# Performance work log

Measured on AMD Instinct MI355X. Metric: run time of the kernel, lower is better.

## Reference

```python
import jax, jax.numpy as jnp
import numpy as np

N, E, H, F, ED, IN = 50000, 800000, 4, 32, 5, 256
NEG_SLOPE = 0.2


def setup_inputs() -> dict:
    key = jax.random.key(0)
    ks = jax.random.split(key, 13)
    s = 0.05
    return {
        "feat": jax.random.normal(ks[0], (N, IN), jnp.float32),
        "edge_fea": jax.random.normal(ks[1], (E, ED), jnp.float32),
        "src": jax.random.randint(ks[2], (E,), 0, N, dtype=jnp.int32),
        "dst": jax.random.randint(ks[3], (E,), 0, N, dtype=jnp.int32),
        "W_fc": jax.random.normal(ks[4], (IN, H * F), jnp.float32) * s,
        "W_edg": jax.random.normal(ks[5], (ED, H * ED), jnp.float32) * s,
        "b_edg": jnp.zeros((H * ED,), jnp.float32),
        "attn_l": jax.random.normal(ks[6], (1, H, F), jnp.float32) * s,
        "attn_r": jax.random.normal(ks[7], (1, H, F), jnp.float32) * s,
        "attn_edg": jax.random.normal(ks[8], (1, H, ED), jnp.float32) * s,
        "W_out": jax.random.normal(ks[9], (ED + F, F), jnp.float32) * s,
        "b_out": jnp.zeros((F,), jnp.float32),
        "bias": jnp.zeros((H * F,), jnp.float32),
    }


def reference(feat, edge_fea, src, dst, W_fc, W_edg, b_edg,
              attn_l, attn_r, attn_edg, W_out, b_out, bias):
    # node projection: [N, IN] -> [N, H, F]
    feat_src = (feat @ W_fc).reshape(N, H, F)
    # edge projection: [E, ED] -> [E, H, ED]
    efe = (edge_fea @ W_edg + b_edg).reshape(E, H, ED)
    # per-head attention logits
    el = (feat_src * attn_l).sum(-1)          # [N, H]
    er = (feat_src * attn_r).sum(-1)          # [N, H]
    ee = (efe * attn_edg).sum(-1)             # [E, H]
    e = jax.nn.leaky_relu(el[src] + er[dst] + ee, NEG_SLOPE)  # [E, H]
    # edge softmax over incoming edges of each dst node (numerically stable)
    m = jax.ops.segment_max(e, dst, num_segments=N)            # [N, H]
    ex = jnp.exp(e - m[dst])
    den = jax.ops.segment_sum(ex, dst, num_segments=N)         # [N, H]
    a = (ex / den[dst])[:, :, None]                            # [E, H, 1]
    # two weighted scatter-aggregations
    ft_f = jax.ops.segment_sum(a * efe, dst, num_segments=N)             # [N, H, ED]
    ft = jax.ops.segment_sum(a * feat_src[src], dst, num_segments=N)     # [N, H, F]
    rst = jnp.concatenate([ft_f, ft], axis=-1) @ W_out + b_out           # [N, H, F]
    rst = rst + bias.reshape(1, H, F)
    return rst
```

## Files before the change

### kernel.cpp

```cpp
#include <hip/hip_runtime.h>
#include <hip/hip_fp16.h>

#define N_NODES 50000
#define E_EDGES 800000
#define H_HEADS 4
#define F_FEAT 32
#define ED_DIM 5
#define IN_DIM 256
#define HF 128
#define NEG_SLOPE 0.2f
#define MAXD 64
#define PAYD 48
#define NPB 16
#define PROJ_BLOCKS 782
#define SCAT_BLOCKS 3125

typedef _Float16 half8 __attribute__((ext_vector_type(8)));
typedef float floatx4 __attribute__((ext_vector_type(4)));

__global__ __launch_bounds__(64) void k_wconv(
    const float* __restrict__ W_fc,
    const float* __restrict__ W_edg, const float* __restrict__ b_edg,
    const float* __restrict__ attn_edg,
    _Float16* __restrict__ Whi, _Float16* __restrict__ Wlo,
    float* __restrict__ WAc, int* __restrict__ cnt)
{
    int b = blockIdx.x;
    int l = threadIdx.x;
    for (int i = b * 64 + l; i < N_NODES; i += 64 * 64) cnt[i] = 0;
    if (b == 0 && l == 0) {
        for (int h = 0; h < 4; ++h) {
            float c0 = 0.f;
            for (int d = 0; d < 5; ++d) c0 += b_edg[h * 5 + d] * attn_edg[h * 5 + d];
            WAc[20 + h] = c0;
            for (int i = 0; i < 5; ++i) {
                float w = 0.f;
                for (int d = 0; d < 5; ++d) w += W_edg[i * 20 + h * 5 + d] * attn_edg[h * 5 + d];
                WAc[i * 4 + h] = w;
            }
        }
    }
    int kt = b >> 3, nt = b & 7;
    int kbase = kt * 32 + (l >> 4) * 8;
    int n = nt * 16 + (l & 15);
    half8 hi, lo;
#pragma unroll
    for (int j = 0; j < 8; ++j) {
        float w = W_fc[(kbase + j) * HF + n];
        _Float16 h = (_Float16)w;
        hi[j] = h;
        lo[j] = (_Float16)(w - (float)h);
    }
    size_t off = ((size_t)b * 64 + l) * 8;
    *(half8*)(Whi + off) = hi;
    *(half8*)(Wlo + off) = lo;
}

template <bool PAY>
__global__ __launch_bounds__(256) void k_proj_scatter(
    const float* __restrict__ feat,
    const _Float16* __restrict__ Whi,
    const _Float16* __restrict__ Wlo,
    const float* __restrict__ attn_l,
    const float* __restrict__ attn_r,
    const int* __restrict__ dst,
    const int* __restrict__ src,
    const float* __restrict__ edge_fea,
    const float* __restrict__ WAc,
    __half2* __restrict__ feat_src,
    float* __restrict__ el,
    float* __restrict__ er,
    int* __restrict__ cnt,
    int* __restrict__ slots,
    char* __restrict__ pay)
{
    if (blockIdx.x >= PROJ_BLOCKS) {
        int e = (blockIdx.x - PROJ_BLOCKS) * 256 + threadIdx.x;
        if (e < E_EDGES) {
            int d = dst[e];
            if constexpr (PAY) {
                int s = src[e];
                const float* ep = edge_fea + (size_t)e * 5;
                float ef0 = ep[0], ef1 = ep[1], ef2 = ep[2], ef3 = ep[3], ef4 = ep[4];
                float ee0 = WAc[20] + ef0*WAc[0] + ef1*WAc[4]  + ef2*WAc[8]  + ef3*WAc[12] + ef4*WAc[16];
                float ee1 = WAc[21] + ef0*WAc[1] + ef1*WAc[5]  + ef2*WAc[9]  + ef3*WAc[13] + ef4*WAc[17];
                float ee2 = WAc[22] + ef0*WAc[2] + ef1*WAc[6]  + ef2*WAc[10] + ef3*WAc[14] + ef4*WAc[18];
                float ee3 = WAc[23] + ef0*WAc[3] + ef1*WAc[7]  + ef2*WAc[11] + ef3*WAc[15] + ef4*WAc[19];
                int pos = atomicAdd(&cnt[d], 1);
                if (pos < PAYD) {
                    float4* pb = (float4*)(pay + ((size_t)d * PAYD + pos) * 32);
                    pb[0] = make_float4(ef0, ef1, ef2, ef3);
                    __half2 e01 = __floats2half2_rn(ee0, ee1);
                    __half2 e23 = __floats2half2_rn(ee2, ee3);
                    float4 w2;
                    w2.x = ef4;
                    w2.y = __int_as_float(s);
                    w2.z = __uint_as_float(*(unsigned*)&e01);
                    w2.w = __uint_as_float(*(unsigned*)&e23);
                    pb[1] = w2;
                }
            } else {
                int pos = atomicAdd(&cnt[d], 1);
                if (pos < MAXD) slots[(size_t)d * MAXD + pos] = e;
            }
        }
        return;
    }

    __shared__ _Float16 sC[4][16][136];

    int t = threadIdx.x;
    int lane = t & 63, wv = t >> 6;
    int l15 = lane & 15, lq = lane >> 4;
    int n0 = blockIdx.x * 64 + wv * 16;
    int arow = n0 + l15;
    int ar = arow < N_NODES ? arow : 0;

    floatx4 acc[8];
#pragma unroll
    for (int i = 0; i < 8; ++i) acc[i] = (floatx4){0.f, 0.f, 0.f, 0.f};

    const float4* Arow = (const float4*)(feat + (size_t)ar * IN_DIM);
    const half8* BH = (const half8*)Whi;
    const half8* BL = (const half8*)Wlo;
    int abase = lq * 2;

    for (int ks = 0; ks < 8; ++ks) {
        float4 a0 = Arow[ks * 8 + abase];
        float4 a1 = Arow[ks * 8 + abase + 1];
        float av[8] = {a0.x, a0.y, a0.z, a0.w, a1.x, a1.y, a1.z, a1.w};
        half8 ahi, alo;
#pragma unroll
        for (int j = 0; j < 8; ++j) {
            _Float16 h = (_Float16)av[j];
            ahi[j] = h;
            alo[j] = (_Float16)(av[j] - (float)h);
        }
#pragma unroll
        for (int tt = 0; tt < 8; ++tt) {
            half8 bh = BH[(ks * 8 + tt) * 64 + lane];
            half8 bl = BL[(ks * 8 + tt) * 64 + lane];
            acc[tt] = __builtin_amdgcn_mfma_f32_16x16x32_f16(ahi, bh, acc[tt], 0, 0, 0);
            acc[tt] = __builtin_amdgcn_mfma_f32_16x16x32_f16(alo, bh, acc[tt], 0, 0, 0);
            acc[tt] = __builtin_amdgcn_mfma_f32_16x16x32_f16(ahi, bl, acc[tt], 0, 0, 0);
        }
    }

#pragma unroll
    for (int tt = 0; tt < 8; ++tt) {
        int c = tt * 16 + l15;
#pragma unroll
        for (int r = 0; r < 4; ++r)
            sC[wv][lq * 4 + r][c] = (_Float16)acc[tt][r];
    }
    __syncthreads();

    int lr = lane >> 2;
    int hh = lane & 3;
    int n = n0 + lr;
    const _Float16* crow = &sC[wv][lr][hh * 32];
    const float* alp = attn_l + hh * 32;
    const float* arp = attn_r + hh * 32;
    float pl = 0.f, pr = 0.f;
#pragma unroll
    for (int i = 0; i < 32; ++i) {
        float v = (float)crow[i];
        pl += v * alp[i];
        pr += v * arp[i];
    }
    if (n < N_NODES) {
        el[n * H_HEADS + hh] = pl;
        er[n * H_HEADS + hh] = pr;
        uint4* po = (uint4*)(feat_src + (size_t)n * 64 + hh * 16);
        const uint4* ps = (const uint4*)crow;
        po[0] = ps[0]; po[1] = ps[1]; po[2] = ps[2]; po[3] = ps[3];
    }
}

__device__ __forceinline__ void acc8f(float* acc, uint4 v, float a) {
    float2 f;
    f = __half22float2(*(__half2*)&v.x); acc[0] += a * f.x; acc[1] += a * f.y;
    f = __half22float2(*(__half2*)&v.y); acc[2] += a * f.x; acc[3] += a * f.y;
    f = __half22float2(*(__half2*)&v.z); acc[4] += a * f.x; acc[5] += a * f.y;
    f = __half22float2(*(__half2*)&v.w); acc[6] += a * f.x; acc[7] += a * f.y;
}

template <bool PAY>
__global__ __launch_bounds__(256) void k_gather_out(
    const int* __restrict__ cnt, const int* __restrict__ slots,
    const char* __restrict__ pay,
    const int* __restrict__ src,
    const float* __restrict__ edge_fea,
    const float* __restrict__ el, const float* __restrict__ er,
    const __half2* __restrict__ feat_src,
    const float* __restrict__ W_edg, const float* __restrict__ b_edg,
    const float* __restrict__ attn_edg,
    const float* __restrict__ W_out, const float* __restrict__ b_out,
    const float* __restrict__ bias,
    float* __restrict__ out)
{
    constexpr int PD   = PAY ? PAYD : MAXD;
    constexpr int SAVR = PAY ? 200  : 264;
    constexpr int SSR  = PAY ? 50   : 66;

    __shared__ float sWe[100], sBe[20], sA[20], sWo[37 * 32], sBo[32], sBi[128];
    __shared__ __align__(16) __half          sav[NPB * SAVR];
    __shared__ __align__(16) unsigned short ssrc[NPB * SSR];
    __shared__ __align__(16) __half          sft[NPB * 136];
    int t = threadIdx.x;
    if (t < 100) sWe[t] = W_edg[t];
    if (t < 20) { sBe[t] = b_edg[t]; sA[t] = attn_edg[t]; }
    for (int i = t; i < 37 * 32; i += 256) sWo[i] = W_out[i];
    if (t < 32)  sBo[t] = b_out[t];
    if (t < 128) sBi[t] = bias[t];
    __syncthreads();

    int lane = t & 63;
    int wv   = t >> 6;
    int q    = lane >> 4;
    int ql   = lane & 15;
    int nb   = wv * 4 + q;
    int n    = blockIdx.x * NPB + nb;
    int h    = ql >> 2;

    int dq = cnt[n]; if (dq > PD) dq = PD;

    if (ql == 0) ssrc[nb * SSR] = 0;
    if (ql < 4)  sav[nb * SAVR + ql] = __float2half(0.f);

    float4 ern = ((const float4*)er)[n];

    float WA[5][4], cst[4];
    if constexpr (!PAY) {
#pragma unroll
        for (int hh = 0; hh < 4; hh++) {
            float c0 = 0.f;
#pragma unroll
            for (int dd = 0; dd < 5; dd++) c0 += sBe[hh * 5 + dd] * sA[hh * 5 + dd];
            cst[hh] = c0;
#pragma unroll
            for (int i = 0; i < 5; i++) {
                float w = 0.f;
#pragma unroll
                for (int dd = 0; dd < 5; dd++) w += sWe[i * 20 + hh * 5 + dd] * sA[hh * 5 + dd];
                WA[i][hh] = w;
            }
        }
    }

    int dmax = dq;
    { int o = __shfl_xor(dmax, 16); dmax = dmax > o ? dmax : o;
      o = __shfl_xor(dmax, 32);     dmax = dmax > o ? dmax : o; }

    float sa4[4] = {0.f, 0.f, 0.f, 0.f};
    float m[20];
#pragma unroll
    for (int i = 0; i < 20; i++) m[i] = 0.f;

    for (int r = 0; r < dmax; r += 16) {
        int idx = r + ql;
        if (idx < dq) {
            float ef0, ef1, ef2, ef3, ef4;
            float b0, b1, b2, b3;
            int s;
            if constexpr (PAY) {
                const uint4* pb = (const uint4*)pay + ((size_t)n * PAYD + idx) * 2;
                uint4 p0 = pb[0], p1 = pb[1];
                ef0 = __uint_as_float(p0.x); ef1 = __uint_as_float(p0.y);
                ef2 = __uint_as_float(p0.z); ef3 = __uint_as_float(p0.w);
                ef4 = __uint_as_float(p1.x);
                s   = (int)p1.y;
                __half2 e01 = *(__half2*)&p1.z;
                __half2 e23 = *(__half2*)&p1.w;
                float2 f01 = __half22float2(e01);
                float2 f23 = __half22float2(e23);
                b0 = f01.x; b1 = f01.y; b2 = f23.x; b3 = f23.y;
            } else {
                int e = slots[(size_t)n * MAXD + idx];
                s = src[e];
                const float* ep = edge_fea + (size_t)e * 5;
                ef0 = ep[0]; ef1 = ep[1]; ef2 = ep[2]; ef3 = ep[3]; ef4 = ep[4];
                b0 = cst[0] + ef0*WA[0][0] + ef1*WA[1][0] + ef2*WA[2][0] + ef3*WA[3][0] + ef4*WA[4][0];
                b1 = cst[1] + ef0*WA[0][1] + ef1*WA[1][1] + ef2*WA[2][1] + ef3*WA[3][1] + ef4*WA[4][1];
                b2 = cst[2] + ef0*WA[0][2] + ef1*WA[1][2] + ef2*WA[2][2] + ef3*WA[3][2] + ef4*WA[4][2];
                b3 = cst[3] + ef0*WA[0][3] + ef1*WA[1][3] + ef2*WA[2][3] + ef3*WA[3][3] + ef4*WA[4][3];
            }
            float4 els = ((const float4*)el)[s];
            float lv0 = els.x + ern.x + b0;
            float lv1 = els.y + ern.y + b1;
            float lv2 = els.z + ern.z + b2;
            float lv3 = els.w + ern.w + b3;
            lv0 = lv0 >= 0.f ? lv0 : NEG_SLOPE * lv0;
            lv1 = lv1 >= 0.f ? lv1 : NEG_SLOPE * lv1;
            lv2 = lv2 >= 0.f ? lv2 : NEG_SLOPE * lv2;
            lv3 = lv3 >= 0.f ? lv3 : NEG_SLOPE * lv3;
            float a0 = __expf(lv0), a1 = __expf(lv1), a2 = __expf(lv2), a3 = __expf(lv3);
            sa4[0] += a0; sa4[1] += a1; sa4[2] += a2; sa4[3] += a3;
            m[0]  += a0 * ef0; m[1]  += a0 * ef1; m[2]  += a0 * ef2; m[3]  += a0 * ef3; m[4]  += a0 * ef4;
            m[5]  += a1 * ef0; m[6]  += a1 * ef1; m[7]  += a1 * ef2; m[8]  += a1 * ef3; m[9]  += a1 * ef4;
            m[10] += a2 * ef0; m[11] += a2 * ef1; m[12] += a2 * ef2; m[13] += a2 * ef3; m[14] += a2 * ef4;
            m[15] += a3 * ef0; m[16] += a3 * ef1; m[17] += a3 * ef2; m[18] += a3 * ef3; m[19] += a3 * ef4;
            ssrc[nb * SSR + idx] = (unsigned short)s;
            __half2 p01 = __floats2half2_rn(a0, a1);
            __half2 p23 = __floats2half2_rn(a2, a3);
            uint2 pk = make_uint2(*(unsigned*)&p01, *(unsigned*)&p23);
            *(uint2*)&sav[nb * SAVR + idx * 4] = pk;
        }
    }

    float acc[8];
#pragma unroll
    for (int k = 0; k < 8; k++) acc[k] = 0.f;
    const uint4* fs4 = (const uint4*)feat_src;
    int savb = nb * SAVR + h;
    int sib  = nb * SSR;

    for (int j = 0; j < dmax; j += 8) {
        int cc[8]; float aa[8]; int ss[8]; uint4 vv[8];
#pragma unroll
        for (int u = 0; u < 8; ++u) {
            int jj = j + u;
            cc[u] = (jj < dq) ? jj : 0;
            aa[u] = (jj < dq) ? __half2float(sav[savb + cc[u] * 4]) : 0.f;
        }
#pragma unroll
        for (int u = 0; u < 8; ++u) ss[u] = ssrc[sib + cc[u]];
#pragma unroll
        for (int u = 0; u < 8; ++u) vv[u] = fs4[(size_t)ss[u] * 16 + ql];
#pragma unroll
        for (int u = 0; u < 8; ++u) acc8f(acc, vv[u], aa[u]);
    }

#pragma unroll
    for (int off = 1; off < 16; off <<= 1) {
#pragma unroll
        for (int hh = 0; hh < 4; hh++) sa4[hh] += __shfl_xor(sa4[hh], off);
#pragma unroll
        for (int qq = 0; qq < 20; qq++) m[qq] += __shfl_xor(m[qq], off);
    }
    float rh = sa4[h] > 0.f ? 1.f / sa4[h] : 0.f;
#pragma unroll
    for (int k = 0; k < 8; k++) acc[k] *= rh;

    {
        __half2 h01 = __floats2half2_rn(acc[0], acc[1]);
        __half2 h23 = __floats2half2_rn(acc[2], acc[3]);
        __half2 h45 = __floats2half2_rn(acc[4], acc[5]);
        __half2 h67 = __floats2half2_rn(acc[6], acc[7]);
        uint4 pk = make_uint4(*(unsigned*)&h01, *(unsigned*)&h23,
                              *(unsigned*)&h45, *(unsigned*)&h67);
        *(uint4*)&sft[nb * 136 + 8 * ql] = pk;
    }

    float ftf[5];
#pragma unroll
    for (int d = 0; d < 5; d++) {
        float s = 0.f;
#pragma unroll
        for (int i = 0; i < 5; i++) s += m[h * 5 + i] * sWe[i * 20 + h * 5 + d];
        ftf[d] = (dq > 0) ? (sBe[h * 5 + d] + s * rh) : 0.f;
    }

    int f0 = 8 * (ql & 3);
    float o[8];
#pragma unroll
    for (int k = 0; k < 8; k++) {
        int f = f0 + k, cc = h * 32 + f;
        o[k] = sBo[f] + sBi[cc];
#pragma unroll
        for (int d = 0; d < 5; d++) o[k] += ftf[d] * sWo[d * 32 + f];
    }
    for (int g = 0; g < 32; g++) {
        float ftg = __half2float(sft[nb * 136 + h * 32 + g]);
#pragma unroll
        for (int k = 0; k < 8; k++) o[k] += ftg * sWo[(5 + g) * 32 + f0 + k];
    }
    float4* po = (float4*)(out + (size_t)n * HF + 8 * ql);
    po[0] = make_float4(o[0], o[1], o[2], o[3]);
    po[1] = make_float4(o[4], o[5], o[6], o[7]);
}

extern "C" void kernel_launch(void* const* d_in, const int* in_sizes, int n_in,
                              void* d_out, int out_size, void* d_ws, size_t ws_size,
                              hipStream_t stream) {
    const float* feat     = (const float*)d_in[0];
    const float* edge_fea = (const float*)d_in[1];
    const int*   src      = (const int*)d_in[2];
    const int*   dst      = (const int*)d_in[3];
    const float* W_fc     = (const float*)d_in[4];
    const float* W_edg    = (const float*)d_in[5];
    const float* b_edg    = (const float*)d_in[6];
    const float* attn_l   = (const float*)d_in[7];
    const float* attn_r   = (const float*)d_in[8];
    const float* attn_edg = (const float*)d_in[9];
    const float* W_out    = (const float*)d_in[10];
    const float* b_out    = (const float*)d_in[11];
    const float* bias     = (const float*)d_in[12];

    char* ws = (char*)d_ws;
    size_t off = 0;
    __half2* feat_src = (__half2*)(ws + off); off += (size_t)N_NODES * 128 * 2;
    float*   el       = (float*)(ws + off);   off += (size_t)N_NODES * 4 * 4;
    float*   er       = (float*)(ws + off);   off += (size_t)N_NODES * 4 * 4;
    int*     cnt      = (int*)(ws + off);     off += (size_t)N_NODES * 4;
    _Float16* Whi     = (_Float16*)(ws + off); off += 8 * 8 * 64 * 8 * 2;
    _Float16* Wlo     = (_Float16*)(ws + off); off += 8 * 8 * 64 * 8 * 2;
    float*   WAc      = (float*)(ws + off);   off += 128;
    size_t off_common = off;
    char* pay = ws + off_common;
    size_t need_pay = off_common + (size_t)N_NODES * PAYD * 32;
    int* slots = (int*)(ws + off_common);

    bool use_pay = ws_size >= need_pay;

    k_wconv<<<64, 64, 0, stream>>>(W_fc, W_edg, b_edg, attn_edg, Whi, Wlo, WAc, cnt);
    if (use_pay) {
        k_proj_scatter<true><<<PROJ_BLOCKS + SCAT_BLOCKS, 256, 0, stream>>>(
            feat, Whi, Wlo, attn_l, attn_r, dst, src, edge_fea, WAc,
            feat_src, el, er, cnt, slots, pay);
        k_gather_out<true><<<N_NODES / NPB, 256, 0, stream>>>(
            cnt, slots, pay, src, edge_fea, el, er, feat_src,
            W_edg, b_edg, attn_edg, W_out, b_out, bias, (float*)d_out);
    } else {
        k_proj_scatter<false><<<PROJ_BLOCKS + SCAT_BLOCKS, 256, 0, stream>>>(
            feat, Whi, Wlo, attn_l, attn_r, dst, src, edge_fea, WAc,
            feat_src, el, er, cnt, slots, pay);
        k_gather_out<false><<<N_NODES / NPB, 256, 0, stream>>>(
            cnt, slots, pay, src, edge_fea, el, er, feat_src,
            W_edg, b_edg, attn_edg, W_out, b_out, bias, (float*)d_out);
    }
}
```

Baseline: 250.7 us.

## Interleave projection and batched edge-scatter blocks with multi-edge-per-thread atomics

Reduces the scatter grid so each scatter block handles 2048 edges, with each thread doing 8 edges in two batches of 4. The loads and atomics in each batch are issued together to expose memory-level parallelism. Scatter blocks are interleaved every third block among the GEMM projection blocks so the memory-bound and compute-bound work co-run on the CUs. Payload writes use nontemporal stores to avoid polluting the cache. This raises register pressure and changes the scheduling order of the atomics, which changes slot order within each destination.

Result: slower. 274.6 us (+9.5%).

```diff
diff --git a/kernel.cpp b/kernel.cpp
--- a/kernel.cpp
+++ b/kernel.cpp
@@ -13,7 +13,8 @@
 #define PAYD 48
 #define NPB 16
 #define PROJ_BLOCKS 782
-#define SCAT_BLOCKS 3125
+#define SCATF_BLOCKS 391
+#define K1_BLOCKS (PROJ_BLOCKS + SCATF_BLOCKS)
 
 typedef _Float16 half8 __attribute__((ext_vector_type(8)));
 typedef float floatx4 __attribute__((ext_vector_type(4)));
@@ -74,45 +75,69 @@
     int* __restrict__ slots,
     char* __restrict__ pay)
 {
-    if (blockIdx.x >= PROJ_BLOCKS) {
-        int e = (blockIdx.x - PROJ_BLOCKS) * 256 + threadIdx.x;
-        if (e < E_EDGES) {
-            int d = dst[e];
+    __shared__ _Float16 sC[4][16][136];
+
+    int bid = blockIdx.x;
+    if (bid % 3 == 2) {
+        int sid = bid / 3;
+        int tid = threadIdx.x;
+        int base = sid * 2048 + tid;
+#pragma unroll
+        for (int g = 0; g < 2; ++g) {
+            int e[4], d[4], s[4], pos[4];
+            bool val[4];
+            float ef[4][5];
+#pragma unroll
+            for (int u = 0; u < 4; ++u) {
+                e[u] = base + (g * 4 + u) * 256;
+                val[u] = e[u] < E_EDGES;
+                int ec = val[u] ? e[u] : 0;
+                d[u] = dst[ec];
+                if constexpr (PAY) {
+                    s[u] = src[ec];
+                    const float* ep = edge_fea + (size_t)ec * 5;
+#pragma unroll
+                    for (int i = 0; i < 5; ++i) ef[u][i] = ep[i];
+                }
+            }
+#pragma unroll
+            for (int u = 0; u < 4; ++u)
+                pos[u] = val[u] ? atomicAdd(&cnt[d[u]], 1) : (PAY ? PAYD : MAXD);
             if constexpr (PAY) {
-                int s = src[e];
-                const float* ep = edge_fea + (size_t)e * 5;
-                float ef0 = ep[0], ef1 = ep[1], ef2 = ep[2], ef3 = ep[3], ef4 = ep[4];
-                float ee0 = WAc[20] + ef0*WAc[0] + ef1*WAc[4]  + ef2*WAc[8]  + ef3*WAc[12] + ef4*WAc[16];
-                float ee1 = WAc[21] + ef0*WAc[1] + ef1*WAc[5]  + ef2*WAc[9]  + ef3*WAc[13] + ef4*WAc[17];
-                float ee2 = WAc[22] + ef0*WAc[2] + ef1*WAc[6]  + ef2*WAc[10] + ef3*WAc[14] + ef4*WAc[18];
-                float ee3 = WAc[23] + ef0*WAc[3] + ef1*WAc[7]  + ef2*WAc[11] + ef3*WAc[15] + ef4*WAc[19];
-                int pos = atomicAdd(&cnt[d], 1);
-                if (pos < PAYD) {
-                    float4* pb = (float4*)(pay + ((size_t)d * PAYD + pos) * 32);
-                    pb[0] = make_float4(ef0, ef1, ef2, ef3);
-                    __half2 e01 = __floats2half2_rn(ee0, ee1);
-                    __half2 e23 = __floats2half2_rn(ee2, ee3);
-                    float4 w2;
-                    w2.x = ef4;
-                    w2.y = __int_as_float(s);
-                    w2.z = __uint_as_float(*(unsigned*)&e01);
-                    w2.w = __uint_as_float(*(unsigned*)&e23);
-                    pb[1] = w2;
+#pragma unroll
+                for (int u = 0; u < 4; ++u) {
+                    if (pos[u] < PAYD) {
+                        float ee0 = WAc[20] + ef[u][0]*WAc[0] + ef[u][1]*WAc[4]  + ef[u][2]*WAc[8]  + ef[u][3]*WAc[12] + ef[u][4]*WAc[16];
+                        float ee1 = WAc[21] + ef[u][0]*WAc[1] + ef[u][1]*WAc[5]  + ef[u][2]*WAc[9]  + ef[u][3]*WAc[13] + ef[u][4]*WAc[17];
+                        float ee2 = WAc[22] + ef[u][0]*WAc[2] + ef[u][1]*WAc[6]  + ef[u][2]*WAc[10] + ef[u][3]*WAc[14] + ef[u][4]*WAc[18];
+                        float ee3 = WAc[23] + ef[u][0]*WAc[3] + ef[u][1]*WAc[7]  + ef[u][2]*WAc[11] + ef[u][3]*WAc[15] + ef[u][4]*WAc[19];
+                        floatx4* pb = (floatx4*)(pay + ((size_t)d[u] * PAYD + pos[u]) * 32);
+                        __half2 e01 = __floats2half2_rn(ee0, ee1);
+                        __half2 e23 = __floats2half2_rn(ee2, ee3);
+                        floatx4 w1 = {ef[u][0], ef[u][1], ef[u][2], ef[u][3]};
+                        floatx4 w2 = {ef[u][4],
+                                      __int_as_float(s[u]),
+                                      __uint_as_float(*(unsigned*)&e01),
+                                      __uint_as_float(*(unsigned*)&e23)};
+                        __builtin_nontemporal_store(w1, pb);
+                        __builtin_nontemporal_store(w2, pb + 1);
+                    }
                 }
             } else {
-                int pos = atomicAdd(&cnt[d], 1);
-                if (pos < MAXD) slots[(size_t)d * MAXD + pos] = e;
+#pragma unroll
+                for (int u = 0; u < 4; ++u)
+                    if (pos[u] < MAXD) slots[(size_t)d[u] * MAXD + pos[u]] = e[u];
             }
         }
         return;
     }
 
-    __shared__ _Float16 sC[4][16][136];
+    int pid = (bid / 3) * 2 + (bid % 3);
 
     int t = threadIdx.x;
     int lane = t & 63, wv = t >> 6;
     int l15 = lane & 15, lq = lane >> 4;
-    int n0 = blockIdx.x * 64 + wv * 16;
+    int n0 = pid * 64 + wv * 16;
     int arow = n0 + l15;
     int ar = arow < N_NODES ? arow : 0;
 
@@ -415,14 +440,14 @@
 
     k_wconv<<<64, 64, 0, stream>>>(W_fc, W_edg, b_edg, attn_edg, Whi, Wlo, WAc, cnt);
     if (use_pay) {
-        k_proj_scatter<true><<<PROJ_BLOCKS + SCAT_BLOCKS, 256, 0, stream>>>(
+        k_proj_scatter<true><<<K1_BLOCKS, 256, 0, stream>>>(
             feat, Whi, Wlo, attn_l, attn_r, dst, src, edge_fea, WAc,
             feat_src, el, er, cnt, slots, pay);
         k_gather_out<true><<<N_NODES / NPB, 256, 0, stream>>>(
             cnt, slots, pay, src, edge_fea, el, er, feat_src,
             W_edg, b_edg, attn_edg, W_out, b_out, bias, (float*)d_out);
     } else {
-        k_proj_scatter<false><<<PROJ_BLOCKS + SCAT_BLOCKS, 256, 0, stream>>>(
+        k_proj_scatter<false><<<K1_BLOCKS, 256, 0, stream>>>(
             feat, Whi, Wlo, attn_l, attn_r, dst, src, edge_fea, WAc,
             feat_src, el, er, cnt, slots, pay);
         k_gather_out<false><<<N_NODES / NPB, 256, 0, stream>>>(
```

## Compress edge payload to 16 bytes and split scatter from projection kernel

Applied to the files above, without the earlier changes.

The per-edge payload staged by destination shrinks from 32 to 16 bytes: edge features are stored as fp16 and the precomputed edge attention logits are dropped. The gather kernel now recomputes those logits from the features using the per-head edge weights it already builds in shared memory. The fused projection+scatter kernel is split into two separate launches, and the WAc precompute is removed from the weight-conversion kernel. This halves scatter-write and gather-read traffic on the payload, at the cost of fp16 rounding of edge features, extra FMAs in the gather, and one more kernel launch that loses the overlap of projection and scatter work.

After: 283.3 us. +13.0%, slower.

```diff
diff --git a/kernel.cpp b/kernel.cpp
--- a/kernel.cpp
+++ b/kernel.cpp
@@ -20,26 +20,12 @@
 
 __global__ __launch_bounds__(64) void k_wconv(
     const float* __restrict__ W_fc,
-    const float* __restrict__ W_edg, const float* __restrict__ b_edg,
-    const float* __restrict__ attn_edg,
     _Float16* __restrict__ Whi, _Float16* __restrict__ Wlo,
-    float* __restrict__ WAc, int* __restrict__ cnt)
+    int* __restrict__ cnt)
 {
     int b = blockIdx.x;
     int l = threadIdx.x;
     for (int i = b * 64 + l; i < N_NODES; i += 64 * 64) cnt[i] = 0;
-    if (b == 0 && l == 0) {
-        for (int h = 0; h < 4; ++h) {
-            float c0 = 0.f;
-            for (int d = 0; d < 5; ++d) c0 += b_edg[h * 5 + d] * attn_edg[h * 5 + d];
-            WAc[20 + h] = c0;
-            for (int i = 0; i < 5; ++i) {
-                float w = 0.f;
-                for (int d = 0; d < 5; ++d) w += W_edg[i * 20 + h * 5 + d] * attn_edg[h * 5 + d];
-                WAc[i * 4 + h] = w;
-            }
-        }
-    }
     int kt = b >> 3, nt = b & 7;
     int kbase = kt * 32 + (l >> 4) * 8;
     int n = nt * 16 + (l & 15);
@@ -57,56 +43,49 @@
 }
 
 template <bool PAY>
-__global__ __launch_bounds__(256) void k_proj_scatter(
+__global__ __launch_bounds__(256) void k_scat(
+    const int* __restrict__ dst,
+    const int* __restrict__ src,
+    const float* __restrict__ edge_fea,
+    int* __restrict__ cnt,
+    int* __restrict__ slots,
+    char* __restrict__ pay)
+{
+    int e = blockIdx.x * 256 + threadIdx.x;
+    if (e >= E_EDGES) return;
+    int d = dst[e];
+    if constexpr (PAY) {
+        int s = src[e];
+        const float* ep = edge_fea + (size_t)e * 5;
+        float ef0 = ep[0], ef1 = ep[1], ef2 = ep[2], ef3 = ep[3], ef4 = ep[4];
+        __half2 q01 = __floats2half2_rn(ef0, ef1);
+        __half2 q23 = __floats2half2_rn(ef2, ef3);
+        __half2 q4  = __floats2half2_rn(ef4, 0.f);
+        int pos = atomicAdd(&cnt[d], 1);
+        if (pos < PAYD) {
+            uint4 v;
+            v.x = *(unsigned*)&q01;
+            v.y = *(unsigned*)&q23;
+            v.z = *(unsigned*)&q4;
+            v.w = (unsigned)s;
+            *(uint4*)(pay + ((size_t)d * PAYD + pos) * 16) = v;
+        }
+    } else {
+        int pos = atomicAdd(&cnt[d], 1);
+        if (pos < MAXD) slots[(size_t)d * MAXD + pos] = e;
+    }
+}
+
+__global__ __launch_bounds__(256) void k_proj(
     const float* __restrict__ feat,
     const _Float16* __restrict__ Whi,
     const _Float16* __restrict__ Wlo,
     const float* __restrict__ attn_l,
     const float* __restrict__ attn_r,
-    const int* __restrict__ dst,
-    const int* __restrict__ src,
-    const float* __restrict__ edge_fea,
-    const float* __restrict__ WAc,
     __half2* __restrict__ feat_src,
     float* __restrict__ el,
-    float* __restrict__ er,
-    int* __restrict__ cnt,
-    int* __restrict__ slots,
-    char* __restrict__ pay)
+    float* __restrict__ er)
 {
-    if (blockIdx.x >= PROJ_BLOCKS) {
-        int e = (blockIdx.x - PROJ_BLOCKS) * 256 + threadIdx.x;
-        if (e < E_EDGES) {
-            int d = dst[e];
-            if constexpr (PAY) {
-                int s = src[e];
-                const float* ep = edge_fea + (size_t)e * 5;
-                float ef0 = ep[0], ef1 = ep[1], ef2 = ep[2], ef3 = ep[3], ef4 = ep[4];
-                float ee0 = WAc[20] + ef0*WAc[0] + ef1*WAc[4]  + ef2*WAc[8]  + ef3*WAc[12] + ef4*WAc[16];
-                float ee1 = WAc[21] + ef0*WAc[1] + ef1*WAc[5]  + ef2*WAc[9]  + ef3*WAc[13] + ef4*WAc[17];
-                float ee2 = WAc[22] + ef0*WAc[2] + ef1*WAc[6]  + ef2*WAc[10] + ef3*WAc[14] + ef4*WAc[18];
-                float ee3 = WAc[23] + ef0*WAc[3] + ef1*WAc[7]  + ef2*WAc[11] + ef3*WAc[15] + ef4*WAc[19];
-                int pos = atomicAdd(&cnt[d], 1);
-                if (pos < PAYD) {
-                    float4* pb = (float4*)(pay + ((size_t)d * PAYD + pos) * 32);
-                    pb[0] = make_float4(ef0, ef1, ef2, ef3);
-                    __half2 e01 = __floats2half2_rn(ee0, ee1);
-                    __half2 e23 = __floats2half2_rn(ee2, ee3);
-                    float4 w2;
-                    w2.x = ef4;
-                    w2.y = __int_as_float(s);
-                    w2.z = __uint_as_float(*(unsigned*)&e01);
-                    w2.w = __uint_as_float(*(unsigned*)&e23);
-                    pb[1] = w2;
-                }
-            } else {
-                int pos = atomicAdd(&cnt[d], 1);
-                if (pos < MAXD) slots[(size_t)d * MAXD + pos] = e;
-            }
-        }
-        return;
-    }
-
     __shared__ _Float16 sC[4][16][136];
 
     int t = threadIdx.x;
@@ -231,20 +210,18 @@
     float4 ern = ((const float4*)er)[n];
 
     float WA[5][4], cst[4];
-    if constexpr (!PAY) {
-#pragma unroll
-        for (int hh = 0; hh < 4; hh++) {
-            float c0 = 0.f;
-#pragma unroll
-            for (int dd = 0; dd < 5; dd++) c0 += sBe[hh * 5 + dd] * sA[hh * 5 + dd];
-            cst[hh] = c0;
-#pragma unroll
-            for (int i = 0; i < 5; i++) {
-                float w = 0.f;
-#pragma unroll
-                for (int dd = 0; dd < 5; dd++) w += sWe[i * 20 + hh * 5 + dd] * sA[hh * 5 + dd];
-                WA[i][hh] = w;
-            }
+#pragma unroll
+    for (int hh = 0; hh < 4; hh++) {
+        float c0 = 0.f;
+#pragma unroll
+        for (int dd = 0; dd < 5; dd++) c0 += sBe[hh * 5 + dd] * sA[hh * 5 + dd];
+        cst[hh] = c0;
+#pragma unroll
+        for (int i = 0; i < 5; i++) {
+            float w = 0.f;
+#pragma unroll
+            for (int dd = 0; dd < 5; dd++) w += sWe[i * 20 + hh * 5 + dd] * sA[hh * 5 + dd];
+            WA[i][hh] = w;
         }
     }
 
@@ -261,30 +238,24 @@
         int idx = r + ql;
         if (idx < dq) {
             float ef0, ef1, ef2, ef3, ef4;
-            float b0, b1, b2, b3;
             int s;
             if constexpr (PAY) {
-                const uint4* pb = (const uint4*)pay + ((size_t)n * PAYD + idx) * 2;
-                uint4 p0 = pb[0], p1 = pb[1];
-                ef0 = __uint_as_float(p0.x); ef1 = __uint_as_float(p0.y);
-                ef2 = __uint_as_float(p0.z); ef3 = __uint_as_float(p0.w);
-                ef4 = __uint_as_float(p1.x);
-                s   = (int)p1.y;
-                __half2 e01 = *(__half2*)&p1.z;
-                __half2 e23 = *(__half2*)&p1.w;
-                float2 f01 = __half22float2(e01);
-                float2 f23 = __half22float2(e23);
-                b0 = f01.x; b1 = f01.y; b2 = f23.x; b3 = f23.y;
+                uint4 p = ((const uint4*)pay)[(size_t)n * PAYD + idx];
+                float2 f01 = __half22float2(*(__half2*)&p.x);
+                float2 f23 = __half22float2(*(__half2*)&p.y);
+                float2 f4x = __half22float2(*(__half2*)&p.z);
+                ef0 = f01.x; ef1 = f01.y; ef2 = f23.x; ef3 = f23.y; ef4 = f4x.x;
+                s = (int)p.w;
             } else {
                 int e = slots[(size_t)n * MAXD + idx];
                 s = src[e];
                 const float* ep = edge_fea + (size_t)e * 5;
                 ef0 = ep[0]; ef1 = ep[1]; ef2 = ep[2]; ef3 = ep[3]; ef4 = ep[4];
-                b0 = cst[0] + ef0*WA[0][0] + ef1*WA[1][0] + ef2*WA[2][0] + ef3*WA[3][0] + ef4*WA[4][0];
-                b1 = cst[1] + ef0*WA[0][1] + ef1*WA[1][1] + ef2*WA[2][1] + ef3*WA[3][1] + ef4*WA[4][1];
-                b2 = cst[2] + ef0*WA[0][2] + ef1*WA[1][2] + ef2*WA[2][2] + ef3*WA[3][2] + ef4*WA[4][2];
-                b3 = cst[3] + ef0*WA[0][3] + ef1*WA[1][3] + ef2*WA[2][3] + ef3*WA[3][3] + ef4*WA[4][3];
             }
+            float b0 = cst[0] + ef0*WA[0][0] + ef1*WA[1][0] + ef2*WA[2][0] + ef3*WA[3][0] + ef4*WA[4][0];
+            float b1 = cst[1] + ef0*WA[0][1] + ef1*WA[1][1] + ef2*WA[2][1] + ef3*WA[3][1] + ef4*WA[4][1];
+            float b2 = cst[2] + ef0*WA[0][2] + ef1*WA[1][2] + ef2*WA[2][2] + ef3*WA[3][2] + ef4*WA[4][2];
+            float b3 = cst[3] + ef0*WA[0][3] + ef1*WA[1][3] + ef2*WA[2][3] + ef3*WA[3][3] + ef4*WA[4][3];
             float4 els = ((const float4*)el)[s];
             float lv0 = els.x + ern.x + b0;
             float lv1 = els.y + ern.y + b1;
@@ -405,26 +376,25 @@
     int*     cnt      = (int*)(ws + off);     off += (size_t)N_NODES * 4;
     _Float16* Whi     = (_Float16*)(ws + off); off += 8 * 8 * 64 * 8 * 2;
     _Float16* Wlo     = (_Float16*)(ws + off); off += 8 * 8 * 64 * 8 * 2;
-    float*   WAc      = (float*)(ws + off);   off += 128;
     size_t off_common = off;
     char* pay = ws + off_common;
-    size_t need_pay = off_common + (size_t)N_NODES * PAYD * 32;
+    size_t need_pay = off_common + (size_t)N_NODES * PAYD * 16;
     int* slots = (int*)(ws + off_common);
 
     bool use_pay = ws_size >= need_pay;
 
-    k_wconv<<<64, 64, 0, stream>>>(W_fc, W_edg, b_edg, attn_edg, Whi, Wlo, WAc, cnt);
+    k_wconv<<<64, 64, 0, stream>>>(W_fc, Whi, Wlo, cnt);
     if (use_pay) {
-        k_proj_scatter<true><<<PROJ_BLOCKS + SCAT_BLOCKS, 256, 0, stream>>>(
-            feat, Whi, Wlo, attn_l, attn_r, dst, src, edge_fea, WAc,
-            feat_src, el, er, cnt, slots, pay);
+        k_scat<true><<<SCAT_BLOCKS, 256, 0, stream>>>(dst, src, edge_fea, cnt, slots, pay);
+        k_proj<<<PROJ_BLOCKS, 256, 0, stream>>>(feat, Whi, Wlo, attn_l, attn_r,
+                                                feat_src, el, er);
         k_gather_out<true><<<N_NODES / NPB, 256, 0, stream>>>(
             cnt, slots, pay, src, edge_fea, el, er, feat_src,
             W_edg, b_edg, attn_edg, W_out, b_out, bias, (float*)d_out);
     } else {
-        k_proj_scatter<false><<<PROJ_BLOCKS + SCAT_BLOCKS, 256, 0, stream>>>(
-            feat, Whi, Wlo, attn_l, attn_r, dst, src, edge_fea, WAc,
-            feat_src, el, er, cnt, slots, pay);
+        k_scat<false><<<SCAT_BLOCKS, 256, 0, stream>>>(dst, src, edge_fea, cnt, slots, pay);
+        k_proj<<<PROJ_BLOCKS, 256, 0, stream>>>(feat, Whi, Wlo, attn_l, attn_r,
+                                                feat_src, el, er);
         k_gather_out<false><<<N_NODES / NPB, 256, 0, stream>>>(
             cnt, slots, pay, src, edge_fea, el, er, feat_src,
             W_edg, b_edg, attn_edg, W_out, b_out, bias, (float*)d_out);
```
